# Optimization experiments

Measured on AMD Instinct MI355X. Metric: run time of the kernel, lower is better.

## Reference

```python
import jax, jax.numpy as jnp
import numpy as np

DIM = 1024
HEADS = 16
HEAD_DIM = 64
INNER = HEADS * HEAD_DIM  # 1024


def setup_inputs() -> dict:
    key = jax.random.key(0)
    ks = jax.random.split(key, 7)
    b, n, m = 2, 2048, 2048
    s = 0.02
    return {
        "x": jax.random.normal(ks[0], (b, n, DIM), dtype=jnp.float32),
        "context": jax.random.normal(ks[1], (b, m, DIM), dtype=jnp.float32),
        "w_kv": jax.random.normal(ks[2], (DIM, 2 * INNER), dtype=jnp.float32) * s,
        "w_q": jax.random.normal(ks[3], (DIM, INNER), dtype=jnp.float32) * s,
        "w_out1": jax.random.normal(ks[4], (INNER, DIM), dtype=jnp.float32) * s,
        "w_out2": jax.random.normal(ks[5], (DIM, DIM), dtype=jnp.float32) * s,
        "gamma": jnp.ones((DIM,), dtype=jnp.float32),
    }


def _split_heads(t):
    # [b, n, h*d] -> [b, h, n, d]
    b, n, _ = t.shape
    return t.reshape(b, n, HEADS, HEAD_DIM).transpose(0, 2, 1, 3)


def reference(x, context, w_kv, w_q, w_out1, w_out2, gamma):
    scale = HEAD_DIM ** -0.5
    kv = context @ w_kv                      # [b, m, 2*inner]
    k, v = jnp.split(kv, 2, axis=-1)
    q = _split_heads(x @ w_q)                # [b, h, n, d]
    k = _split_heads(k)                      # [b, h, m, d]
    v = _split_heads(v)
    dots = jnp.einsum('bhid,bhjd->bhij', q, k) * scale
    attn = jax.nn.softmax(dots, axis=-1)
    out = jnp.einsum('bhij,bhjd->bhid', attn, v)
    b, h, n, d = out.shape
    out = out.transpose(0, 2, 1, 3).reshape(b, n, h * d)   # [b, n, inner]
    out = jax.nn.relu(out @ w_out1) @ w_out2               # to_out MLP (dropout off)
    # AttnLayerNorm: layer_norm over last dim with gamma, beta=0
    mean = jnp.mean(out, axis=-1, keepdims=True)
    var = jnp.var(out, axis=-1, keepdims=True)
    return (out - mean) * jax.lax.rsqrt(var + 1e-5) * gamma
```

## Files before the change

kernel.cpp:

```cpp
#include <hip/hip_runtime.h>
#include <hip/hip_bf16.h>

typedef unsigned short u16;
typedef unsigned int u32;
typedef __attribute__((ext_vector_type(4))) float f32x4;
typedef __attribute__((ext_vector_type(16))) float f32x16;
typedef __attribute__((ext_vector_type(8))) __bf16 bf16x8;

constexpr int kDim   = 1024;
constexpr int kSeq   = 2048;
constexpr int kB     = 2;
constexpr int kHeads = 16;
constexpr int kRows  = kB * kSeq;

__device__ __forceinline__ u16 f2bf(float f) {
  __hip_bfloat16 h = __float2bfloat16(f);
  return __builtin_bit_cast(u16, h);
}

__device__ __forceinline__ u32 pkbf(float a, float b) {
  return (u32)f2bf(a) | ((u32)f2bf(b) << 16);
}

__device__ __forceinline__ u32 cvtpk(float lo, float hi) {
  u32 r;
  asm("v_cvt_pk_bf16_f32 %0, %1, %2" : "=v"(r) : "v"(lo), "v"(hi));
  return r;
}

__device__ __forceinline__ float exp2x(float x) {
#if __has_builtin(__builtin_amdgcn_exp2f)
  return __builtin_amdgcn_exp2f(x);
#else
  return exp2f(x);
#endif
}

__device__ __forceinline__ void plswap(u32& a, u32& b) {
  asm volatile("v_permlane32_swap_b32 %0, %1" : "+v"(a), "+v"(b));
}

__device__ __forceinline__ float xsum32(float x) {
  return x + __shfl_xor(x, 32);
}

__device__ __forceinline__ void gload_lds16(const void* src, void* dst) {
  __builtin_amdgcn_global_load_lds(
      (const __attribute__((address_space(1))) void*)src,
      (__attribute__((address_space(3))) void*)dst, 16, 0, 0);
}

__device__ __forceinline__ f32x4 mfma16(bf16x8 a, bf16x8 b, f32x4 c) {
  return __builtin_amdgcn_mfma_f32_16x16x32_bf16(a, b, c, 0, 0, 0);
}

__device__ __forceinline__ f32x16 mfma32(bf16x8 a, bf16x8 b, f32x16 c) {
  return __builtin_amdgcn_mfma_f32_32x32x16_bf16(a, b, c, 0, 0, 0);
}

__device__ __forceinline__ void convert_body(const float* __restrict__ in,
                                             u16* __restrict__ out, int n4,
                                             int vbid, int nblk) {
  int i = vbid * 256 + threadIdx.x;
  const int stride = nblk * 256;
  for (; i < n4; i += stride) {
    float4 v = ((const float4*)in)[i];
    ushort4 o;
    o.x = f2bf(v.x); o.y = f2bf(v.y); o.z = f2bf(v.z); o.w = f2bf(v.w);
    ((ushort4*)out)[i] = o;
  }
}

__device__ __forceinline__ void transpose_tile(const float* __restrict__ in,
                                               u16* __restrict__ out, int K, int N,
                                               int bx, int by, float (*tile)[33]) {
  const int tx = threadIdx.x & 31;
  const int ty = threadIdx.x >> 5;
  const int k0 = by * 32;
  const int n0 = bx * 32;
#pragma unroll
  for (int i = 0; i < 4; ++i)
    tile[ty + i * 8][tx] = in[(size_t)(k0 + ty + i * 8) * N + n0 + tx];
  __syncthreads();
#pragma unroll
  for (int i = 0; i < 4; ++i)
    out[(size_t)(n0 + ty + i * 8) * K + k0 + tx] = f2bf(tile[tx][ty + i * 8]);
}

__global__ __launch_bounds__(256) void prep_kernel(
    const float* __restrict__ x,   u16* __restrict__ xb,
    const float* __restrict__ ctx, u16* __restrict__ cb,
    const float* __restrict__ wkv, u16* __restrict__ wkvT,
    const float* __restrict__ wq,  u16* __restrict__ wqT,
    const float* __restrict__ w1,  u16* __restrict__ w1T,
    const float* __restrict__ w2,  u16* __restrict__ w2T) {
  __shared__ float tile[32][33];
  int bid = blockIdx.x;
  if (bid < 2048) { transpose_tile(wkv, wkvT, 1024, 2048, bid & 63, bid >> 6, tile); return; }
  bid -= 2048;
  if (bid < 1024) { transpose_tile(wq, wqT, 1024, 1024, bid & 31, bid >> 5, tile); return; }
  bid -= 1024;
  if (bid < 1024) { transpose_tile(w1, w1T, 1024, 1024, bid & 31, bid >> 5, tile); return; }
  bid -= 1024;
  if (bid < 1024) { transpose_tile(w2, w2T, 1024, 1024, bid & 31, bid >> 5, tile); return; }
  bid -= 1024;
  if (bid < 1024) { convert_body(x, xb, kRows * 1024 / 4, bid, 1024); return; }
  bid -= 1024;
  convert_body(ctx, cb, kRows * 1024 / 4, bid, 1024);
}

template <int EPI, int TN>
__device__ __forceinline__ void gemm_body(const u16* __restrict__ A,
                                          const u16* __restrict__ Bt,
                                          void* __restrict__ out0,
                                          void* __restrict__ out1, int N,
                                          int m0, int n0,
                                          u16* ldsA, u16* ldsB) {
  constexpr int K  = 1024;
  constexpr int WN = (TN == 128) ? 2 : 1;
  constexpr int WM = 4 / WN;
  constexpr int MF = 128 / WM / 16;
  constexpr int NF = TN / WN / 16;
  constexpr int NCHUNK = 16 + TN / 8;
  constexpr int CPW = NCHUNK / 4;
  const int tid  = threadIdx.x;
  const int lane = tid & 63;
  const int wave = tid >> 6;
  const int wm = wave / WN, wn = wave % WN;

  f32x4 acc[MF][NF];
#pragma unroll
  for (int i = 0; i < MF; ++i)
#pragma unroll
    for (int j = 0; j < NF; ++j) acc[i][j] = (f32x4)0.f;

  const int srow = lane >> 3;
  const int sslt = lane & 7;

  for (int kt = 0; kt < K / 64; ++kt) {
    const int k0 = kt * 64;
#pragma unroll
    for (int i = 0; i < CPW; ++i) {
      const int c = wave * CPW + i;
      if (c < 16) {
        const int row = c * 8 + srow;
        const int cb  = sslt ^ (row & 7);
        gload_lds16(A + (size_t)(m0 + row) * K + k0 + cb * 8, ldsA + c * 512);
      } else {
        const int cc  = c - 16;
        const int row = cc * 8 + srow;
        const int cb  = sslt ^ (row & 7);
        gload_lds16(Bt + (size_t)(n0 + row) * K + k0 + cb * 8, ldsB + cc * 512);
      }
    }
    __syncthreads();
#pragma unroll
    for (int ks = 0; ks < 2; ++ks) {
      const int kb = (ks * 32 + (lane >> 4) * 8) >> 3;
      bf16x8 af[MF], bfr[NF];
#pragma unroll
      for (int mf = 0; mf < MF; ++mf) {
        const int row = wm * (128 / WM) + mf * 16 + (lane & 15);
        af[mf] = *(const bf16x8*)(ldsA + row * 64 + (kb ^ (row & 7)) * 8);
      }
#pragma unroll
      for (int nf = 0; nf < NF; ++nf) {
        const int row = wn * (TN / WN) + nf * 16 + (lane & 15);
        bfr[nf] = *(const bf16x8*)(ldsB + row * 64 + (kb ^ (row & 7)) * 8);
      }
#pragma unroll
      for (int mf = 0; mf < MF; ++mf)
#pragma unroll
        for (int nf = 0; nf < NF; ++nf)
          acc[mf][nf] = mfma16(af[mf], bfr[nf], acc[mf][nf]);
    }
    __syncthreads();
  }

  const int rb = (lane >> 4) * 4;
  const int cc = lane & 15;
#pragma unroll
  for (int mf = 0; mf < MF; ++mf)
#pragma unroll
    for (int nf = 0; nf < NF; ++nf)
#pragma unroll
      for (int r = 0; r < 4; ++r) {
        const int grow = m0 + wm * (128 / WM) + mf * 16 + rb + r;
        const int gcol = n0 + wn * (TN / WN) + nf * 16 + cc;
        const float v = acc[mf][nf][r];
        if constexpr (EPI == 1) {
          ((u16*)out0)[(size_t)grow * N + gcol] = f2bf(v * 0.18033688f);
        } else {
          const int b = grow >> 11, m = grow & 2047;
          if (gcol < 1024) {
            ((u16*)out0)[(size_t)grow * 1024 + gcol] = f2bf(v);
          } else {
            const int df = gcol - 1024;
            const int h = df >> 6, d = df & 63;
            ((u16*)out1)[(((size_t)(b * kHeads + h) * 64 + d) << 11) + m] = f2bf(v);
          }
        }
      }
}

__global__ __launch_bounds__(256, 3) void gemm_kvq(const u16* __restrict__ cb,
                                                   const u16* __restrict__ wkvT,
                                                   u16* __restrict__ kbuf,
                                                   u16* __restrict__ vT,
                                                   const u16* __restrict__ xb,
                                                   const u16* __restrict__ wqT,
                                                   u16* __restrict__ qbuf) {
  __shared__ u16 ldsA[128 * 64];
  __shared__ u16 ldsB[128 * 64];
  const int swz = (blockIdx.x & 7) * 128 + (blockIdx.x >> 3);
  const int chunk = swz >> 7, off = swz & 127;
  if (off < 64) {
    const int bid = chunk * 64 + off;
    gemm_body<4, 128>(cb, wkvT, kbuf, vT, 2048,
                      (bid >> 4) * 128, (bid & 15) * 128, ldsA, ldsB);
  } else {
    const int bid = chunk * 64 + (off - 64);
    gemm_body<1, 64>(xb, wqT, qbuf, nullptr, 1024,
                     (bid >> 4) * 128, (bid & 15) * 64, ldsA, ldsB);
  }
}

template <int EPI>
__global__ __launch_bounds__(256, 4) void gemm64(const u16* __restrict__ A,
                                                 const u16* __restrict__ Bt,
                                                 void* __restrict__ out0, int N) {
  constexpr int K = 1024;
  __shared__ u16 ldsA[2][64 * 64];
  __shared__ u16 ldsB[2][64 * 64];
  const int lane = threadIdx.x & 63;
  const int wave = threadIdx.x >> 6;
  const int l31  = lane & 31;
  const int hi   = lane >> 5;
  const int wm = wave >> 1, wn = wave & 1;

  const int swz = (blockIdx.x & 7) * 128 + (blockIdx.x >> 3);
  const int m0 = (swz >> 4) * 64;
  const int n0 = (swz & 15) * 64;

  f32x16 acc = (f32x16)0.f;

  const int srow = lane >> 3, sslt = lane & 7;
  const int arow = wm * 32 + l31;
  const int brow = wn * 32 + l31;
  const int asw = arow & 7, bsw = brow & 7;

  auto stage = [&](int buf, int kt) {
    const int k0 = kt * 64;
#pragma unroll
    for (int j = 0; j < 4; ++j) {
      const int c = wave * 4 + j;
      const int row = (c & 7) * 8 + srow;
      const int cb  = sslt ^ (row & 7);
      if (c < 8)
        gload_lds16(A + (size_t)(m0 + row) * K + k0 + cb * 8, ldsA[buf] + (c & 7) * 512);
      else
        gload_lds16(Bt + (size_t)(n0 + row) * K + k0 + cb * 8, ldsB[buf] + (c & 7) * 512);
    }
  };

  stage(0, 0);
  for (int kt = 0; kt < K / 64; ++kt) {
    __syncthreads();
    const int cur = kt & 1;
    if (kt + 1 < K / 64) stage(cur ^ 1, kt + 1);
#pragma unroll
    for (int ks = 0; ks < 4; ++ks) {
      bf16x8 af = *(const bf16x8*)(ldsA[cur] + arow * 64 + ((2 * ks + hi) ^ asw) * 8);
      bf16x8 bf = *(const bf16x8*)(ldsB[cur] + brow * 64 + ((2 * ks + hi) ^ bsw) * 8);
      acc = mfma32(af, bf, acc);
    }
  }

#pragma unroll
  for (int r = 0; r < 16; ++r) {
    const int grow = m0 + wm * 32 + (r & 3) + 8 * (r >> 2) + 4 * hi;
    const int gcol = n0 + wn * 32 + l31;
    const float v = acc[r];
    if constexpr (EPI == 2) {
      ((u16*)out0)[(size_t)grow * N + gcol] = f2bf(v > 0.f ? v : 0.f);
    } else {
      ((float*)out0)[(size_t)grow * N + gcol] = v;
    }
  }
}

__global__ __launch_bounds__(512, 4) void attn_kernel(const u16* __restrict__ Q,
                                                      const u16* __restrict__ Kb,
                                                      const u16* __restrict__ Vt,
                                                      u16* __restrict__ O) {
  __shared__ __align__(16) unsigned char smem[65536];

  const int swz = (blockIdx.x & 7) * 64 + (blockIdx.x >> 3);
  const int qt = swz & 15;
  const int bh = swz >> 4;
  const int h = bh & 15, b = bh >> 4;

  const int tid  = threadIdx.x;
  const int lane = tid & 63;
  const int wave = tid >> 6;
  const int kw   = wave & 1;
  const int qw   = wave >> 1;
  const int l32  = lane & 31;
  const int hi   = lane >> 5;
  const int q0   = qt * 128 + qw * 32;

  const u16* qp = Q + (size_t)(b * kSeq + q0 + l32) * 1024 + h * 64 + hi * 8;
  bf16x8 bq[4];
#pragma unroll
  for (int ks = 0; ks < 4; ++ks) bq[ks] = *(const bf16x8*)(qp + ks * 16);

  f32x16 acc[2];
  acc[0] = (f32x16)0.f; acc[1] = (f32x16)0.f;
  float l_ = 0.f;

  const int srow = lane >> 3, sslt = lane & 7;

  auto stage_pair = [&](int dbuf, int kvbase) {
    u16* baseK = (u16*)(smem + dbuf * 32768);
    u16* baseV = (u16*)(smem + dbuf * 32768 + 16384);
#pragma unroll
    for (int j = 0; j < 4; ++j) {
      const int c = wave * 4 + j;
      if (c < 16) {
        const int par = c >> 3, cc = c & 7;
        const int row = cc * 8 + srow;
        const int cb  = sslt ^ (row & 7);
        gload_lds16(Kb + (size_t)(b * kSeq + kvbase + par * 64 + row) * 1024 +
                        h * 64 + cb * 8,
                    baseK + par * 4096 + cc * 512);
      } else {
        const int cv = c - 16, par = cv >> 3, cc = cv & 7;
        const int row = cc * 8 + srow;
        const int cb  = sslt ^ (row & 7);
        gload_lds16(Vt + (size_t)((b * kHeads + h) * 64 + row) * kSeq +
                        kvbase + par * 64 + cb * 8,
                    baseV + par * 4096 + cc * 512);
      }
    }
  };

  stage_pair(0, 0);

  for (int it = 0; it < kSeq / 128; ++it) {
    __syncthreads();
    const int cur = it & 1;
    if (it + 1 < kSeq / 128) stage_pair(cur ^ 1, (it + 1) * 128);

    const u16* myK = (const u16*)(smem + cur * 32768) + kw * 4096;
    const u16* myV = (const u16*)(smem + cur * 32768 + 16384) + kw * 4096;

#pragma unroll
    for (int kvt = 0; kvt < 2; ++kvt) {
      const int krow = kvt * 32 + l32;
      const int ksw  = krow & 7;
      bf16x8 kf[4];
#pragma unroll
      for (int ks = 0; ks < 4; ++ks)
        kf[ks] = *(const bf16x8*)(&myK[krow * 64 + ((2 * ks + hi) ^ ksw) * 8]);
      f32x16 s = (f32x16)0.f;
#pragma unroll
      for (int ks = 0; ks < 4; ++ks) s = mfma32(kf[ks], bq[ks], s);

#pragma unroll
      for (int r = 0; r < 16; ++r) s[r] = exp2x(s[r]);
      const float t0 = (s[0] + s[1]) + (s[2] + s[3]);
      const float t1 = (s[4] + s[5]) + (s[6] + s[7]);
      const float t2 = (s[8] + s[9]) + (s[10] + s[11]);
      const float t3 = (s[12] + s[13]) + (s[14] + s[15]);
      l_ += (t0 + t1) + (t2 + t3);

      u32 w[8];
#pragma unroll
      for (int p = 0; p < 8; ++p) w[p] = cvtpk(s[2 * p], s[2 * p + 1]);
      plswap(w[0], w[2]); plswap(w[1], w[3]);
      plswap(w[4], w[6]); plswap(w[5], w[7]);
      union { u32 u[4]; bf16x8 v; } f0, f1;
      f0.u[0] = w[0]; f0.u[1] = w[1]; f0.u[2] = w[2]; f0.u[3] = w[3];
      f1.u[0] = w[4]; f1.u[1] = w[5]; f1.u[2] = w[6]; f1.u[3] = w[7];

#pragma unroll
      for (int nd = 0; nd < 2; ++nd) {
        const int vrow = nd * 32 + l32;
        const int vsw  = vrow & 7;
        bf16x8 v0 = *(const bf16x8*)(&myV[vrow * 64 + ((4 * kvt + hi) ^ vsw) * 8]);
        bf16x8 v1 = *(const bf16x8*)(&myV[vrow * 64 + ((4 * kvt + 2 + hi) ^ vsw) * 8]);
        acc[nd] = mfma32(v0, f0.v, acc[nd]);
        acc[nd] = mfma32(v1, f1.v, acc[nd]);
      }
    }
  }

  __syncthreads();
  float* mg = (float*)smem;
  if (kw == 1) {
    float* mp = mg + (qw * 64 + lane) * 33;
#pragma unroll
    for (int r = 0; r < 16; ++r) { mp[r] = acc[0][r]; mp[16 + r] = acc[1][r]; }
    mp[32] = l_;
  }
  __syncthreads();
  if (kw == 0) {
    const float* mp = mg + (qw * 64 + lane) * 33;
#pragma unroll
    for (int r = 0; r < 16; ++r) { acc[0][r] += mp[r]; acc[1][r] += mp[16 + r]; }
    l_ += mp[32];

    const float inv = 1.f / xsum32(l_);
    const size_t rowb = (size_t)(b * kSeq + q0 + l32) * 1024 + h * 64;
#pragma unroll
    for (int nd = 0; nd < 2; ++nd)
#pragma unroll
      for (int r4 = 0; r4 < 4; ++r4) {
        uint2 o;
        o.x = pkbf(acc[nd][4 * r4 + 0] * inv, acc[nd][4 * r4 + 1] * inv);
        o.y = pkbf(acc[nd][4 * r4 + 2] * inv, acc[nd][4 * r4 + 3] * inv);
        *(uint2*)(O + rowb + nd * 32 + r4 * 8 + hi * 4) = o;
      }
  }
}

__global__ __launch_bounds__(256) void ln_kernel(float* __restrict__ io,
                                                 const float* __restrict__ gamma) {
  const int row = blockIdx.x;
  float* p = io + (size_t)row * 1024;
  float4 v = ((const float4*)p)[threadIdx.x];
  float s  = v.x + v.y + v.z + v.w;
  float ss = v.x * v.x + v.y * v.y + v.z * v.z + v.w * v.w;
#pragma unroll
  for (int m = 1; m < 64; m <<= 1) {
    s  += __shfl_xor(s, m);
    ss += __shfl_xor(ss, m);
  }
  __shared__ float red[8];
  const int wave = threadIdx.x >> 6, lane = threadIdx.x & 63;
  if (lane == 0) { red[wave] = s; red[4 + wave] = ss; }
  __syncthreads();
  s  = red[0] + red[1] + red[2] + red[3];
  ss = red[4] + red[5] + red[6] + red[7];
  const float mean = s * (1.f / 1024.f);
  const float var  = ss * (1.f / 1024.f) - mean * mean;
  const float rr   = rsqrtf(var + 1e-5f);
  float4 g = ((const float4*)gamma)[threadIdx.x];
  v.x = (v.x - mean) * rr * g.x;
  v.y = (v.y - mean) * rr * g.y;
  v.z = (v.z - mean) * rr * g.z;
  v.w = (v.w - mean) * rr * g.w;
  ((float4*)p)[threadIdx.x] = v;
}

extern "C" void kernel_launch(void* const* d_in, const int* in_sizes, int n_in,
                              void* d_out, int out_size, void* d_ws, size_t ws_size,
                              hipStream_t stream) {
  const float* x      = (const float*)d_in[0];
  const float* ctx    = (const float*)d_in[1];
  const float* w_kv   = (const float*)d_in[2];
  const float* w_q    = (const float*)d_in[3];
  const float* w_out1 = (const float*)d_in[4];
  const float* w_out2 = (const float*)d_in[5];
  const float* gamma  = (const float*)d_in[6];

  char* ws = (char*)d_ws;
  size_t off = 0;
  auto alloc = [&](size_t bytes) {
    void* p = ws + off;
    off += (bytes + 255) & ~(size_t)255;
    return p;
  };
  u16* xb   = (u16*)alloc((size_t)kRows * 1024 * 2);
  u16* cb   = (u16*)alloc((size_t)kRows * 1024 * 2);
  u16* wkvT = (u16*)alloc((size_t)2048 * 1024 * 2);
  u16* wqT  = (u16*)alloc((size_t)1024 * 1024 * 2);
  u16* w1T  = (u16*)alloc((size_t)1024 * 1024 * 2);
  u16* w2T  = (u16*)alloc((size_t)1024 * 1024 * 2);
  u16* kbuf = (u16*)alloc((size_t)kRows * 1024 * 2);
  u16* vT   = (u16*)alloc((size_t)kRows * 1024 * 2);
  u16* qbuf = (u16*)alloc((size_t)kRows * 1024 * 2);
  u16* attno  = cb;
  u16* hidden = xb;

  prep_kernel<<<7168, 256, 0, stream>>>(x, xb, ctx, cb, w_kv, wkvT, w_q, wqT,
                                        w_out1, w1T, w_out2, w2T);
  gemm_kvq<<<1024, 256, 0, stream>>>(cb, wkvT, kbuf, vT, xb, wqT, qbuf);
  attn_kernel<<<512, 512, 0, stream>>>(qbuf, kbuf, vT, attno);
  gemm64<2><<<1024, 256, 0, stream>>>(attno, w1T, hidden, 1024);
  gemm64<3><<<1024, 256, 0, stream>>>(hidden, w2T, d_out, 1024);
  ln_kernel<<<kRows, 256, 0, stream>>>((float*)d_out, gamma);
}
```

Baseline: 129.3 us.

## Double-buffer the KV/Q projection GEMM with a BK=32 LDS pipeline

Restructures the fused KV/Q projection GEMM body to use two LDS buffers with a K-tile of 32. Each buffer gets a matching 4-slot XOR swizzle. The next K tile is prefetched into the alternate buffer before the MFMAs on the current one run, so each iteration needs one barrier instead of two. This is meant to overlap global-to-LDS loads with compute, at the cost of twice as many loop iterations with fewer MFMAs each. The gemm64 kernels are only renamed.

New measurement: 138.7 us. +7.3%, slower.

```diff
diff --git a/kernel.cpp b/kernel.cpp
--- a/kernel.cpp
+++ b/kernel.cpp
@@ -110,19 +110,22 @@
 }
 
 template <int EPI, int TN>
-__device__ __forceinline__ void gemm_body(const u16* __restrict__ A,
-                                          const u16* __restrict__ Bt,
-                                          void* __restrict__ out0,
-                                          void* __restrict__ out1, int N,
-                                          int m0, int n0,
-                                          u16* ldsA, u16* ldsB) {
+__device__ __forceinline__ void gemm128_body(const u16* __restrict__ A,
+                                             const u16* __restrict__ Bt,
+                                             void* __restrict__ out0,
+                                             void* __restrict__ out1, int N,
+                                             int m0, int n0,
+                                             u16* ldsA, u16* ldsB) {
   constexpr int K  = 1024;
   constexpr int WN = (TN == 128) ? 2 : 1;
   constexpr int WM = 4 / WN;
   constexpr int MF = 128 / WM / 16;
   constexpr int NF = TN / WN / 16;
-  constexpr int NCHUNK = 16 + TN / 8;
-  constexpr int CPW = NCHUNK / 4;
+  constexpr int ACH = 8;
+  constexpr int BCH = TN / 16;
+  constexpr int CPW = (ACH + BCH + 3) / 4;
+  constexpr int ABUF = 128 * 32;
+  constexpr int BBUF = TN * 32;
   const int tid  = threadIdx.x;
   const int lane = tid & 63;
   const int wave = tid >> 6;
@@ -134,47 +137,54 @@
 #pragma unroll
     for (int j = 0; j < NF; ++j) acc[i][j] = (f32x4)0.f;
 
-  const int srow = lane >> 3;
-  const int sslt = lane & 7;
-
-  for (int kt = 0; kt < K / 64; ++kt) {
-    const int k0 = kt * 64;
+  const int srow = lane >> 2;
+  const int sslt = lane & 3;
+
+  auto stage = [&](int buf, int kt) {
+    const int k0 = kt * 32;
 #pragma unroll
     for (int i = 0; i < CPW; ++i) {
       const int c = wave * CPW + i;
-      if (c < 16) {
-        const int row = c * 8 + srow;
-        const int cb  = sslt ^ (row & 7);
-        gload_lds16(A + (size_t)(m0 + row) * K + k0 + cb * 8, ldsA + c * 512);
-      } else {
-        const int cc  = c - 16;
-        const int row = cc * 8 + srow;
-        const int cb  = sslt ^ (row & 7);
-        gload_lds16(Bt + (size_t)(n0 + row) * K + k0 + cb * 8, ldsB + cc * 512);
+      if (c < ACH) {
+        const int row = c * 16 + srow;
+        const int cb  = sslt ^ ((row >> 1) & 3);
+        gload_lds16(A + (size_t)(m0 + row) * K + k0 + cb * 8,
+                    ldsA + buf * ABUF + c * 512);
+      } else if (c < ACH + BCH) {
+        const int cc  = c - ACH;
+        const int row = cc * 16 + srow;
+        const int cb  = sslt ^ ((row >> 1) & 3);
+        gload_lds16(Bt + (size_t)(n0 + row) * K + k0 + cb * 8,
+                    ldsB + buf * BBUF + cc * 512);
       }
     }
+  };
+
+  const int kb = lane >> 4;
+  stage(0, 0);
+  for (int kt = 0; kt < K / 32; ++kt) {
     __syncthreads();
-#pragma unroll
-    for (int ks = 0; ks < 2; ++ks) {
-      const int kb = (ks * 32 + (lane >> 4) * 8) >> 3;
-      bf16x8 af[MF], bfr[NF];
-#pragma unroll
-      for (int mf = 0; mf < MF; ++mf) {
-        const int row = wm * (128 / WM) + mf * 16 + (lane & 15);
-        af[mf] = *(const bf16x8*)(ldsA + row * 64 + (kb ^ (row & 7)) * 8);
-      }
-#pragma unroll
-      for (int nf = 0; nf < NF; ++nf) {
-        const int row = wn * (TN / WN) + nf * 16 + (lane & 15);
-        bfr[nf] = *(const bf16x8*)(ldsB + row * 64 + (kb ^ (row & 7)) * 8);
-      }
-#pragma unroll
-      for (int mf = 0; mf < MF; ++mf)
-#pragma unroll
-        for (int nf = 0; nf < NF; ++nf)
-          acc[mf][nf] = mfma16(af[mf], bfr[nf], acc[mf][nf]);
-    }
-    __syncthreads();
+    const int cur = kt & 1;
+    if (kt + 1 < K / 32) stage(cur ^ 1, kt + 1);
+
+    bf16x8 af[MF], bfr[NF];
+#pragma unroll
+    for (int mf = 0; mf < MF; ++mf) {
+      const int row = wm * (128 / WM) + mf * 16 + (lane & 15);
+      af[mf] = *(const bf16x8*)(ldsA + cur * ABUF + row * 32 +
+                                (kb ^ ((row >> 1) & 3)) * 8);
+    }
+#pragma unroll
+    for (int nf = 0; nf < NF; ++nf) {
+      const int row = wn * (TN / WN) + nf * 16 + (lane & 15);
+      bfr[nf] = *(const bf16x8*)(ldsB + cur * BBUF + row * 32 +
+                                 (kb ^ ((row >> 1) & 3)) * 8);
+    }
+#pragma unroll
+    for (int mf = 0; mf < MF; ++mf)
+#pragma unroll
+      for (int nf = 0; nf < NF; ++nf)
+        acc[mf][nf] = mfma16(af[mf], bfr[nf], acc[mf][nf]);
   }
 
   const int rb = (lane >> 4) * 4;
@@ -210,25 +220,25 @@
                                                    const u16* __restrict__ xb,
                                                    const u16* __restrict__ wqT,
                                                    u16* __restrict__ qbuf) {
-  __shared__ u16 ldsA[128 * 64];
-  __shared__ u16 ldsB[128 * 64];
+  __shared__ u16 ldsA[2 * 128 * 32];
+  __shared__ u16 ldsB[2 * 128 * 32];
   const int swz = (blockIdx.x & 7) * 128 + (blockIdx.x >> 3);
   const int chunk = swz >> 7, off = swz & 127;
   if (off < 64) {
     const int bid = chunk * 64 + off;
-    gemm_body<4, 128>(cb, wkvT, kbuf, vT, 2048,
-                      (bid >> 4) * 128, (bid & 15) * 128, ldsA, ldsB);
+    gemm128_body<4, 128>(cb, wkvT, kbuf, vT, 2048,
+                         (bid >> 4) * 128, (bid & 15) * 128, ldsA, ldsB);
   } else {
     const int bid = chunk * 64 + (off - 64);
-    gemm_body<1, 64>(xb, wqT, qbuf, nullptr, 1024,
-                     (bid >> 4) * 128, (bid & 15) * 64, ldsA, ldsB);
+    gemm128_body<1, 64>(xb, wqT, qbuf, nullptr, 1024,
+                        (bid >> 4) * 128, (bid & 15) * 64, ldsA, ldsB);
   }
 }
 
 template <int EPI>
-__global__ __launch_bounds__(256, 4) void gemm64(const u16* __restrict__ A,
-                                                 const u16* __restrict__ Bt,
-                                                 void* __restrict__ out0, int N) {
+__global__ __launch_bounds__(256, 4) void gemm64k(const u16* __restrict__ A,
+                                                  const u16* __restrict__ Bt,
+                                                  void* __restrict__ out0, int N) {
   constexpr int K = 1024;
   __shared__ u16 ldsA[2][64 * 64];
   __shared__ u16 ldsB[2][64 * 64];
@@ -487,7 +497,7 @@
                                         w_out1, w1T, w_out2, w2T);
   gemm_kvq<<<1024, 256, 0, stream>>>(cb, wkvT, kbuf, vT, xb, wqT, qbuf);
   attn_kernel<<<512, 512, 0, stream>>>(qbuf, kbuf, vT, attno);
-  gemm64<2><<<1024, 256, 0, stream>>>(attno, w1T, hidden, 1024);
-  gemm64<3><<<1024, 256, 0, stream>>>(hidden, w2T, d_out, 1024);
+  gemm64k<2><<<1024, 256, 0, stream>>>(attno, w1T, hidden, 1024);
+  gemm64k<3><<<1024, 256, 0, stream>>>(hidden, w2T, d_out, 1024);
   ln_kernel<<<kRows, 256, 0, stream>>>((float*)d_out, gamma);
 }
```
